# Kernel tuning notes

Hardware: AMD Instinct MI355X
Metric: run time of the kernel (lower is better)

The kernel has to match this reference:

```python
import jax, jax.numpy as jnp
import numpy as np

B, S, WD, H, STEP = 32, 512, 512, 512, 2
NG = 8  # gate order: f1, f2, f3, f4, f5, i, o, u


def setup_inputs() -> dict:
    key = jax.random.key(0)
    ks = jax.random.split(key, 12)
    std = 0.1
    word_inputs = jax.random.normal(ks[0], (B, S, WD), jnp.float32)
    position_table = jax.random.randint(ks[1], (B, S), 0, S + 1)  # 0 -> pad row
    mask = jnp.ones((B, S), jnp.int32)
    # nograd uniform(-0.05, 0.05) initial states created inside torch forward
    init_h = jax.random.uniform(ks[2], (B, S, H), jnp.float32, -0.05, 0.05)
    init_c = jax.random.uniform(ks[3], (B, S, H), jnp.float32, -0.05, 0.05)
    Wx = std * jax.random.normal(ks[4], (NG, H, H), jnp.float32)
    Wh = std * jax.random.normal(ks[5], (NG, 2 * H, H), jnp.float32)
    Wi = std * jax.random.normal(ks[6], (NG, WD, H), jnp.float32)
    Wd = std * jax.random.normal(ks[7], (NG, H, H), jnp.float32)
    Ws = std * jax.random.normal(ks[8], (NG, H, H), jnp.float32)
    b = std * jax.random.normal(ks[9], (NG, H), jnp.float32)
    gW = std * jax.random.normal(ks[10], (6, H, H), jnp.float32)  # Wxd,Whd,Wxo,Who,Wxf,Whf
    gb = std * jax.random.normal(ks[11], (3, H), jnp.float32)     # bd,bo,bf
    return dict(word_inputs=word_inputs, init_h=init_h, init_c=init_c,
                Wx=Wx, Wh=Wh, Wi=Wi, Wd=Wd, Ws=Ws, b=b, gW=gW, gb=gb,
                position_table=position_table, mask=mask, num_layers=4)


def _shift_sum_before(x, steps):
    # sum_{s=1..steps} of x right-shifted by s with zero padding at front
    out = jnp.zeros_like(x)
    for s in range(1, steps + 1):
        pad = jnp.zeros(x[:, :s].shape, x.dtype)
        out = out + jnp.concatenate([pad, x[:, :-s]], axis=1)
    return out


def _shift_sum_after(x, steps):
    out = jnp.zeros_like(x)
    for s in range(1, steps + 1):
        pad = jnp.zeros(x[:, :s].shape, x.dtype)
        out = out + jnp.concatenate([x[:, s:], pad], axis=1)
    return out


def _position_switch(x, pos):
    # prepend a zero pad row at position 0, then gather along seq dim
    x_add = jnp.concatenate([jnp.zeros_like(x[:, :1]), x], axis=1)  # [B,S+1,H]
    return jnp.take_along_axis(x_add, pos[:, :, None], axis=1)


def reference(word_inputs, init_h, init_c, Wx, Wh, Wi, Wd, Ws, b, gW, gb,
              position_table, mask, num_layers):
    maskf = mask.astype(jnp.float32)
    seq_mask = maskf[:, :, None]                         # [B,S,1]
    mask_score = (maskf * 1e25 - 1e25)[:, :, None]       # 0 where valid, -1e25 where pad
    emb = (word_inputs * seq_mask).reshape(-1, WD)       # embedding_hidden_state_pre
    h = init_h * seq_mask
    c = init_c * seq_mask
    dummy_h = jnp.mean(h, axis=1)
    dummy_c = jnp.mean(c, axis=1)
    gWxd, gWhd, gWxo, gWho, gWxf, gWhf = gW[0], gW[1], gW[2], gW[3], gW[4], gW[5]
    gbd, gbo, gbf = gb[0], gb[1], gb[2]
    for _ in range(num_layers):
        sw_h = _position_switch(h, position_table)
        sw_c = _position_switch(c, position_table)
        combined = jnp.mean(h, axis=1)                   # [B,H]
        rh = h.reshape(-1, H)                            # [B*S,H]
        td_h = jnp.broadcast_to(dummy_h[:, None], h.shape).reshape(-1, H)
        # dummy (sentence-state) node update
        gd = jax.nn.sigmoid(dummy_h @ gWxd + combined @ gWhd + gbd)
        go = jax.nn.sigmoid(dummy_h @ gWxo + combined @ gWho + gbo)
        gf = jax.nn.sigmoid(td_h @ gWxf + rh @ gWhf + gbf).reshape(h.shape) + mask_score
        scores = jax.nn.softmax(jnp.concatenate([gf, gd[:, None]], axis=1), axis=1)  # [B,S+1,H]
        dummy_c_new = jnp.sum(scores[:, :S] * c, axis=1) + scores[:, S] * dummy_c
        dummy_h_new = go * jnp.tanh(dummy_c_new)
        # neighbor window sums (before/after) for h and c
        hb = _shift_sum_before(h, STEP).reshape(-1, H)
        ha = _shift_sum_after(h, STEP).reshape(-1, H)
        cb = _shift_sum_before(c, STEP).reshape(-1, H)
        ca = _shift_sum_after(c, STEP).reshape(-1, H)
        cat = jnp.concatenate([hb, ha], axis=1)          # [B*S,2H]
        td_c = jnp.broadcast_to(dummy_c[:, None], c.shape).reshape(-1, H)
        sw_hf = sw_h.reshape(-1, H)
        sw_cf = sw_c.reshape(-1, H)
        # all 8 gate pre-activations in stacked einsums: [8,B*S,H]
        z = (jnp.einsum('nh,ghk->gnk', rh, Wx)
             + jnp.einsum('nd,gdk->gnk', cat, Wh)
             + jnp.einsum('nw,gwk->gnk', emb, Wi)
             + jnp.einsum('nh,ghk->gnk', td_h, Wd)
             + jnp.einsum('nh,ghk->gnk', sw_hf, Ws)
             + b[:, None, :])
        gates6 = jax.nn.softmax(jax.nn.sigmoid(z[:6]), axis=0)  # normalize f1..f5,i
        f1, f2, f3, f4, f5, i_t = gates6[0], gates6[1], gates6[2], gates6[3], gates6[4], gates6[5]
        o_t = jax.nn.sigmoid(z[6])
        u_t = jnp.tanh(z[7])
        cf = c.reshape(-1, H)
        c_new = f1 * cb + f2 * ca + f3 * cf + f4 * td_c + f5 * sw_cf + i_t * u_t
        h_new = o_t * jnp.tanh(c_new)
        h = h_new.reshape(B, S, H) * seq_mask
        c = c_new.reshape(B, S, H) * seq_mask
        dummy_h, dummy_c = dummy_h_new, dummy_c_new
    return h
```

## Files before the change

### kernel.cpp

```cpp
#include <hip/hip_runtime.h>
#include <cstddef>

#define Bn 32
#define Sn 512
#define Hn 512
#define Rn (Bn*Sn)
#define NLAYER 4
constexpr size_t NHe = (size_t)Rn * Hn;

typedef __attribute__((ext_vector_type(8))) _Float16 f16x8;
typedef __attribute__((ext_vector_type(4))) float f32x4;

__device__ __forceinline__ float sigf(float x) { return 1.f / (1.f + __expf(-x)); }
__device__ __forceinline__ void gl_lds16(const void* g, void* l) {
  __builtin_amdgcn_global_load_lds((const __attribute__((address_space(1))) void*)g,
                                   (__attribute__((address_space(3))) void*)l, 16, 0, 0);
}
#define VMCNT(n) asm volatile("s_waitcnt vmcnt(" #n ")" ::: "memory")

__device__ __forceinline__ int a32slot(int b, int k) {
  int kcT = k >> 5, quad = (k >> 3) & 3, j = k & 7, rg = b >> 4, l15 = b & 15;
  return ((((kcT * 2 + rg) * 4 + quad) * 16 + l15) * 8) + j;
}

__global__ void k_init(const float* __restrict__ ih, const float* __restrict__ ic,
                       const int* __restrict__ mask,
                       float* __restrict__ h, float* __restrict__ c) {
  size_t i = (size_t)blockIdx.x * blockDim.x + threadIdx.x;
  size_t n = i >> 7;
  float m = (float)mask[n];
  float4 b = ((const float4*)ih)[i];
  float4 d = ((const float4*)ic)[i];
  b.x *= m; b.y *= m; b.z *= m; b.w *= m;
  d.x *= m; d.y *= m; d.z *= m; d.w *= m;
  ((float4*)h)[i] = b; ((float4*)c)[i] = d;
}

__global__ void k_mean2(const float* __restrict__ x, const float* __restrict__ y,
                        _Float16* __restrict__ dh16, float* __restrict__ oy) {
  int idx = blockIdx.x * blockDim.x + threadIdx.x;
  int b = idx >> 9, k = idx & 511;
  const float* px = x + (size_t)b * Sn * Hn + k;
  const float* py = y + (size_t)b * Sn * Hn + k;
  float sx = 0.f, sy = 0.f;
#pragma unroll 8
  for (int t = 0; t < Sn; ++t) { sx += px[(size_t)t * Hn]; sy += py[(size_t)t * Hn]; }
  oy[idx] = sy * (1.f / Sn);
  dh16[a32slot(b, k)] = (_Float16)(sx * (1.f / Sn));
}

__global__ void k_mean1a(const float* __restrict__ x, float* __restrict__ part) {
  int b = blockIdx.x, sc = blockIdx.y;
  int k4 = threadIdx.x & 127;
  int so = threadIdx.x >> 7;
  const float4* px = (const float4*)x + ((size_t)(b * Sn + sc * 64 + so)) * 128 + k4;
  float4 s = make_float4(0.f, 0.f, 0.f, 0.f);
#pragma unroll 4
  for (int t = 0; t < 32; ++t) {
    float4 v = px[(size_t)t * 256];
    s.x += v.x; s.y += v.y; s.z += v.z; s.w += v.w;
  }
  ((float4*)part)[((size_t)(sc * 2 + so) * Bn + b) * 128 + k4] = s;
}
__global__ void k_mean1b(const float* __restrict__ part, _Float16* __restrict__ comb16) {
  int idx = blockIdx.x * blockDim.x + threadIdx.x;
  int b = idx >> 7, k4 = idx & 127;
  float4 s = make_float4(0.f, 0.f, 0.f, 0.f);
#pragma unroll
  for (int p = 0; p < 16; ++p) {
    float4 v = ((const float4*)part)[((size_t)p * Bn + b) * 128 + k4];
    s.x += v.x; s.y += v.y; s.z += v.z; s.w += v.w;
  }
  float vv[4] = {s.x, s.y, s.z, s.w};
#pragma unroll
  for (int jj = 0; jj < 4; ++jj)
    comb16[a32slot(b, k4 * 4 + jj)] = (_Float16)(vv[jj] * (1.f / Sn));
}

__global__ void k_convS(const float* __restrict__ gW, const float* __restrict__ Wd,
                        _Float16* __restrict__ Shat) {
  int kcT = blockIdx.x, nT4 = blockIdx.y, mat = blockIdx.z;
  int tid = threadIdx.x;
  const float* w = (mat < 5) ? (gW + (size_t)mat * 262144)
                             : (Wd + (size_t)(mat - 5) * 262144);
  size_t sb = ((size_t)((mat * 4 + nT4) * 16 + kcT)) * 4096;
#pragma unroll
  for (int half = 0; half < 2; ++half) {
    int st = half * 256 + tid;
    int nj = st >> 6, quad = (st >> 4) & 3, l15 = st & 15;
    int n = nT4 * 128 + nj * 16 + l15;
    int k0 = kcT * 32 + quad * 8;
    f16x8 w8;
#pragma unroll
    for (int j = 0; j < 8; ++j) w8[j] = (_Float16)w[(size_t)(k0 + j) * Hn + n];
    *(f16x8*)&Shat[sb + (size_t)st * 8] = w8;
  }
}

__global__ __launch_bounds__(256) void k_small(const _Float16* __restrict__ dh16,
                                               const _Float16* __restrict__ comb16,
                                               const _Float16* __restrict__ Shat,
                                               float* __restrict__ S) {
  const int mat = blockIdx.x, nT4 = blockIdx.y;
  const int tid = threadIdx.x;
  const int lane = tid & 63, wid = tid >> 6;
  const int quad = lane >> 4, l15 = lane & 15;
  const _Float16* A16 = (mat == 1 || mat == 3) ? comb16 : dh16;
  const _Float16* Sb = Shat + ((size_t)((mat * 4 + nT4) * 16)) * 4096;

  f32x4 acc[2][2];
#pragma unroll
  for (int rg = 0; rg < 2; ++rg)
#pragma unroll
    for (int nj = 0; nj < 2; ++nj) acc[rg][nj] = (f32x4){0.f, 0.f, 0.f, 0.f};

#pragma unroll 4
  for (int kcT = 0; kcT < 16; ++kcT) {
    f16x8 a0 = *(const f16x8*)&A16[(((kcT * 2 + 0) * 4 + quad) * 16 + l15) * 8];
    f16x8 a1 = *(const f16x8*)&A16[(((kcT * 2 + 1) * 4 + quad) * 16 + l15) * 8];
    f16x8 b0 = *(const f16x8*)&Sb[(size_t)kcT * 4096 + (((wid * 2 + 0) * 4 + quad) * 16 + l15) * 8];
    f16x8 b1 = *(const f16x8*)&Sb[(size_t)kcT * 4096 + (((wid * 2 + 1) * 4 + quad) * 16 + l15) * 8];
    acc[0][0] = __builtin_amdgcn_mfma_f32_16x16x32_f16(a0, b0, acc[0][0], 0, 0, 0);
    acc[0][1] = __builtin_amdgcn_mfma_f32_16x16x32_f16(a0, b1, acc[0][1], 0, 0, 0);
    acc[1][0] = __builtin_amdgcn_mfma_f32_16x16x32_f16(a1, b0, acc[1][0], 0, 0, 0);
    acc[1][1] = __builtin_amdgcn_mfma_f32_16x16x32_f16(a1, b1, acc[1][1], 0, 0, 0);
  }
#pragma unroll
  for (int rg = 0; rg < 2; ++rg)
#pragma unroll
    for (int nj = 0; nj < 2; ++nj)
#pragma unroll
      for (int r = 0; r < 4; ++r) {
        int brow = rg * 16 + quad * 4 + r;
        int col = nT4 * 128 + (wid * 2 + nj) * 16 + l15;
        S[(size_t)mat * 16384 + brow * 512 + col] = acc[rg][nj][r];
      }
}

__global__ void k_gates2(const float* __restrict__ S, const float* __restrict__ gb,
                         float* __restrict__ gd, float* __restrict__ go,
                         float* __restrict__ gfA) {
  int idx = blockIdx.x * blockDim.x + threadIdx.x;
  int k = idx & 511;
  gd[idx] = sigf(S[idx] + S[16384 + idx] + gb[k]);
  go[idx] = sigf(S[2 * 16384 + idx] + S[3 * 16384 + idx] + gb[512 + k]);
  gfA[idx] = S[4 * 16384 + idx] + gb[1024 + k];
}

__global__ void k_dummy2(const float* __restrict__ pnum, const float* __restrict__ pden,
                         const float* __restrict__ gd, const float* __restrict__ go,
                         const float* __restrict__ dc,
                         _Float16* __restrict__ dh16o, float* __restrict__ dc2) {
  int idx = blockIdx.x * blockDim.x + threadIdx.x;
  int b = idx >> 9, k = idx & 511;
  float ed = __expf(gd[idx]);
  float num = ed * dc[idx], den = ed;
#pragma unroll
  for (int q = 0; q < 4; ++q) {
    num += pnum[(size_t)(b * 4 + q) * 512 + k];
    den += pden[(size_t)(b * 4 + q) * 512 + k];
  }
  float d = num / den;
  dc2[idx] = d;
  dh16o[a32slot(b, k)] = (_Float16)(go[idx] * tanhf(d));
}

__global__ void k_convw(const float* __restrict__ Wx, const float* __restrict__ Wh,
                        const float* __restrict__ Wsm, const float* __restrict__ Wi,
                        _Float16* __restrict__ Bhat) {
  int kcT = blockIdx.x, nT = blockIdx.y, tg = blockIdx.z;
  int t = tg >> 3, g = tg & 7;
  const float* base;
  if (t == 0)      base = Wx  + (size_t)g * 262144;
  else if (t == 1) base = Wh  + (size_t)g * 524288;
  else if (t == 2) base = Wh  + (size_t)g * 524288 + 262144;
  else if (t == 3) base = Wsm + (size_t)g * 262144;
  else             base = Wi  + (size_t)g * 262144;
  size_t sbase = ((size_t)(t * 16 + nT) * 16 + kcT) * 8192 + (size_t)g * 1024;
  int lane = threadIdx.x;
  for (int cch = lane; cch < 128; cch += 64) {
    int ni = cch >> 6, quad = (cch >> 4) & 3, l15 = cch & 15;
    int n = nT * 32 + ni * 16 + l15;
    int k0 = kcT * 32 + quad * 8;
    f16x8 w8;
#pragma unroll
    for (int j = 0; j < 8; ++j) w8[j] = (_Float16)base[(size_t)(k0 + j) * Hn + n];
    *(f16x8*)&Bhat[sbase + (size_t)cch * 8] = w8;
  }
}

__global__ void k_convG(const float* __restrict__ gW, _Float16* __restrict__ Ghat) {
  int kcT = blockIdx.x, nT4 = blockIdx.y;
  int tid = threadIdx.x;
  const float* w = gW + (size_t)5 * Hn * Hn;
  size_t sb = ((size_t)(nT4 * 16 + kcT)) * 4096;
#pragma unroll
  for (int half = 0; half < 2; ++half) {
    int st = half * 256 + tid;
    int nj = st >> 6, quad = (st >> 4) & 3, l15 = st & 15;
    int n = nT4 * 128 + nj * 16 + l15;
    int k0 = kcT * 32 + quad * 8;
    f16x8 w8;
#pragma unroll
    for (int j = 0; j < 8; ++j) w8[j] = (_Float16)w[(size_t)(k0 + j) * Hn + n];
    *(f16x8*)&Ghat[sb + (size_t)st * 8] = w8;
  }
}

__global__ void k_prepAll(const float* __restrict__ h, const int* __restrict__ pos,
                          _Float16* __restrict__ Ahat) {
  const int mb = blockIdx.x, kcT = blockIdx.y;
  const int tid = threadIdx.x;
#pragma unroll
  for (int half = 0; half < 2; ++half) {
    int st = half * 256 + tid;
    int rg = st >> 6, quad = (st >> 4) & 3, l15 = st & 15;
    int r = mb * 128 + rg * 16 + l15;
    int srow = r & (Sn - 1);
    int k0 = kcT * 32 + quad * 8;
    const float* base = h + (size_t)r * Hn + k0;
    float v0[8], v1[8], v2[8], v3[8];
#pragma unroll
    for (int j = 0; j < 8; ++j) { v0[j] = base[j]; v1[j] = 0.f; v2[j] = 0.f; v3[j] = 0.f; }
    if (srow >= 1) { const float* p = base - Hn;
#pragma unroll
      for (int j = 0; j < 8; ++j) v1[j] += p[j]; }
    if (srow >= 2) { const float* p = base - 2 * Hn;
#pragma unroll
      for (int j = 0; j < 8; ++j) v1[j] += p[j]; }
    if (srow <= Sn - 2) { const float* p = base + Hn;
#pragma unroll
      for (int j = 0; j < 8; ++j) v2[j] += p[j]; }
    if (srow <= Sn - 3) { const float* p = base + 2 * Hn;
#pragma unroll
      for (int j = 0; j < 8; ++j) v2[j] += p[j]; }
    int pp = pos[r];
    if (pp) {
      const float* p = h + ((size_t)((r >> 9) * Sn + pp - 1)) * Hn + k0;
#pragma unroll
      for (int j = 0; j < 8; ++j) v3[j] = p[j];
    }
    size_t stoff = (size_t)st * 8;
    f16x8 o0, o1, o2, o3;
#pragma unroll
    for (int j = 0; j < 8; ++j) {
      o0[j] = (_Float16)v0[j]; o1[j] = (_Float16)v1[j];
      o2[j] = (_Float16)v2[j]; o3[j] = (_Float16)v3[j];
    }
    *(f16x8*)&Ahat[((size_t)(0 * 128 + mb) * 16 + kcT) * 4096 + stoff] = o0;
    *(f16x8*)&Ahat[((size_t)(1 * 128 + mb) * 16 + kcT) * 4096 + stoff] = o1;
    *(f16x8*)&Ahat[((size_t)(2 * 128 + mb) * 16 + kcT) * 4096 + stoff] = o2;
    *(f16x8*)&Ahat[((size_t)(3 * 128 + mb) * 16 + kcT) * 4096 + stoff] = o3;
  }
}

__global__ void k_prepW(const float* __restrict__ w, const int* __restrict__ mask,
                        _Float16* __restrict__ Ahat) {
  const int mb = blockIdx.x, kcT = blockIdx.y;
  const int tid = threadIdx.x;
  size_t sb = ((size_t)(4 * 128 + mb) * 16 + kcT) * 4096;
#pragma unroll
  for (int half = 0; half < 2; ++half) {
    int st = half * 256 + tid;
    int rg = st >> 6, quad = (st >> 4) & 3, l15 = st & 15;
    int r = mb * 128 + rg * 16 + l15;
    int k0 = kcT * 32 + quad * 8;
    float mf = (float)mask[r];
    const float* base = w + (size_t)r * Hn + k0;
    f16x8 o8;
#pragma unroll
    for (int j = 0; j < 8; ++j) o8[j] = (_Float16)(base[j] * mf);
    *(f16x8*)&Ahat[sb + (size_t)st * 8] = o8;
  }
}

__global__ __launch_bounds__(256, 2) void k_gemm1d(const _Float16* __restrict__ Ahat,
                                                   const _Float16* __restrict__ Ghat,
                                                   const float* __restrict__ gfA,
                                                   const float* __restrict__ cbuf,
                                                   const int* __restrict__ mask,
                                                   float* __restrict__ pnum,
                                                   float* __restrict__ pden) {
  __shared__ _Float16 As[2][4096];
  __shared__ _Float16 Bs[2][4096];
  __shared__ float red[4][2][128];
  const int tid = threadIdx.x;
  const int mb = blockIdx.x, nT4 = blockIdx.y;
  const int lane = tid & 63, wid = tid >> 6;
  const int quad = lane >> 4, l15 = lane & 15;
  const int afo0 = (((wid * 2 + 0) * 4 + quad) * 16 + l15) * 8;
  const int afo1 = (((wid * 2 + 1) * 4 + quad) * 16 + l15) * 8;

  f32x4 acc[2][8];
#pragma unroll
  for (int mi = 0; mi < 2; ++mi)
#pragma unroll
    for (int nj = 0; nj < 8; ++nj) acc[mi][nj] = (f32x4){0.f, 0.f, 0.f, 0.f};

  auto stage = [&](int buf, int kcT) {
    const int4* sa = (const int4*)Ahat + ((size_t)(mb * 16 + kcT) << 9);
    const int4* sbp = (const int4*)Ghat + ((size_t)(nT4 * 16 + kcT) << 9);
#pragma unroll
    for (int q = 0; q < 2; ++q) {
      gl_lds16(sa + q * 256 + tid, &As[buf][(q * 256 + tid) * 8]);
      gl_lds16(sbp + q * 256 + tid, &Bs[buf][(q * 256 + tid) * 8]);
    }
  };

  stage(0, 0);
  __syncthreads();
#pragma unroll 1
  for (int kcT = 0; kcT < 16; ++kcT) {
    const int cur = kcT & 1;
    if (kcT < 15) stage(cur ^ 1, kcT + 1);
    f16x8 a0 = *(const f16x8*)&As[cur][afo0];
    f16x8 a1 = *(const f16x8*)&As[cur][afo1];
#pragma unroll
    for (int nj = 0; nj < 8; ++nj) {
      f16x8 bh = *(const f16x8*)&Bs[cur][((nj * 4 + quad) * 16 + l15) * 8];
      acc[0][nj] = __builtin_amdgcn_mfma_f32_16x16x32_f16(a0, bh, acc[0][nj], 0, 0, 0);
      acc[1][nj] = __builtin_amdgcn_mfma_f32_16x16x32_f16(a1, bh, acc[1][nj], 0, 0, 0);
    }
    __syncthreads();
  }

  const int bb = mb >> 2;
  float gfa[8], nsum[8], dsum[8];
#pragma unroll
  for (int nj = 0; nj < 8; ++nj) {
    gfa[nj] = gfA[bb * 512 + nT4 * 128 + nj * 16 + l15];
    nsum[nj] = 0.f; dsum[nj] = 0.f;
  }
#pragma unroll
  for (int mi = 0; mi < 2; ++mi) {
#pragma unroll
    for (int r = 0; r < 4; ++r) {
      int row = mb * 128 + wid * 32 + mi * 16 + quad * 4 + r;
      float mf = (float)mask[row];
      const float* crow = cbuf + (size_t)row * 512 + nT4 * 128 + l15;
#pragma unroll
      for (int nj = 0; nj < 8; ++nj) {
        float e = __expf(sigf(acc[mi][nj][r] + gfa[nj])) * mf;
        nsum[nj] += e * crow[nj * 16];
        dsum[nj] += e;
      }
    }
  }
#pragma unroll
  for (int nj = 0; nj < 8; ++nj) {
    nsum[nj] += __shfl_xor(nsum[nj], 16);
    nsum[nj] += __shfl_xor(nsum[nj], 32);
    dsum[nj] += __shfl_xor(dsum[nj], 16);
    dsum[nj] += __shfl_xor(dsum[nj], 32);
  }
  if (quad == 0) {
#pragma unroll
    for (int nj = 0; nj < 8; ++nj) {
      red[wid][0][nj * 16 + l15] = nsum[nj];
      red[wid][1][nj * 16 + l15] = dsum[nj];
    }
  }
  __syncthreads();
  {
    int cc = tid & 127, which = tid >> 7;
    float v = red[0][which][cc] + red[1][which][cc] + red[2][which][cc] + red[3][which][cc];
    float* dst = which ? pden : pnum;
    dst[(size_t)mb * 512 + nT4 * 128 + cc] = v;
  }
}

__global__ __launch_bounds__(512, 2) void k_mega(
    const float* __restrict__ c,
    const _Float16* __restrict__ Ahat, const _Float16* __restrict__ Bhat,
    const int* __restrict__ pos, const int* __restrict__ mask,
    const float* __restrict__ dc, const float* __restrict__ dWd,
    const float* __restrict__ bias,
    float* __restrict__ hout, float* __restrict__ cout) {
  __shared__ _Float16 As[2][16384];
  __shared__ _Float16 Bs[2][16384];

  const int tid = threadIdx.x;
  const int id = blockIdx.x;
  const int xcd = id & 7;
  const int loc = id >> 3;
  const int mt = xcd * 8 + (loc >> 4);
  const int nT = loc & 15;
  const int m0 = mt * 256;
  const int n0 = nT * 32;
  const int bb = m0 >> 9;

  const int lane = tid & 63, wid = tid >> 6;
  const int quad = lane >> 4, l15 = lane & 15;
  const int row_grp = wid >> 1;
  const int col_half = wid & 1;
  const int mb2 = row_grp >> 1;
  const int rg0 = (row_grp & 1) * 4;

  const int afoA0 = (mb2 * 4096) + ((rg0 * 4 + quad) * 16 + l15) * 8;
  const int afoA1 = (2 * 4096 + mb2 * 4096) + ((rg0 * 4 + quad) * 16 + l15) * 8;
  const int bfo = col_half * 512 + quad * 128 + l15 * 8;

  f32x4 acc[8][4];
#pragma unroll
  for (int g = 0; g < 8; ++g)
#pragma unroll
    for (int mi = 0; mi < 4; ++mi) acc[g][mi] = (f32x4){0.f, 0.f, 0.f, 0.f};

  auto stageA = [&](int buf, int kt2) {
    const int t = kt2 >> 3, kc2 = (kt2 & 7) * 2;
#pragma unroll
    for (int kk = 0; kk < 2; ++kk)
#pragma unroll
      for (int m2 = 0; m2 < 2; ++m2) {
        const int4* src = (const int4*)Ahat +
            ((size_t)((t * 128 + mt * 2 + m2) * 16 + kc2 + kk)) * 512;
        gl_lds16(src + tid, &As[buf][(kk * 2 + m2) * 4096 + tid * 8]);
      }
#pragma unroll
    for (int kk = 0; kk < 2; ++kk) {
      const int4* srcb = (const int4*)Bhat +
          ((size_t)((t * 16 + nT) * 16 + kc2 + kk)) * 1024;
      gl_lds16(srcb + tid, &Bs[buf][kk * 8192 + tid * 8]);
    }
  };
  auto stageB = [&](int buf, int kt2) {
    const int t = kt2 >> 3, kc2 = (kt2 & 7) * 2;
#pragma unroll
    for (int kk = 0; kk < 2; ++kk) {
      const int4* srcb = (const int4*)Bhat +
          ((size_t)((t * 16 + nT) * 16 + kc2 + kk)) * 1024 + 512;
      gl_lds16(srcb + tid, &Bs[buf][kk * 8192 + 4096 + tid * 8]);
    }
  };

  stageA(0, 0);
  stageB(0, 0);

#pragma unroll 1
  for (int kt = 0; kt < 40; ++kt) {
    const int cur = kt & 1;
    const int nbuf = cur ^ 1;
    VMCNT(2);
    __builtin_amdgcn_s_barrier();
    f16x8 a[4][2], b[4];
#pragma unroll
    for (int mi = 0; mi < 4; ++mi) {
      a[mi][0] = *(const f16x8*)&As[cur][afoA0 + mi * 512];
      a[mi][1] = *(const f16x8*)&As[cur][afoA1 + mi * 512];
    }
#pragma unroll
    for (int g = 0; g < 4; ++g) b[g] = *(const f16x8*)&Bs[cur][g * 1024 + bfo];
    if (kt < 39) stageA(nbuf, kt + 1);
    asm volatile("s_waitcnt lgkmcnt(0)" ::: "memory");
    __builtin_amdgcn_sched_barrier(0);
    __builtin_amdgcn_s_setprio(1);
#pragma unroll
    for (int g = 0; g < 4; ++g) {
#pragma unroll
      for (int mi = 0; mi < 4; ++mi)
        acc[g][mi] = __builtin_amdgcn_mfma_f32_16x16x32_f16(a[mi][0], b[g], acc[g][mi], 0, 0, 0);
    }
    f16x8 b1[4];
#pragma unroll
    for (int g = 0; g < 4; ++g) b1[g] = *(const f16x8*)&Bs[cur][8192 + g * 1024 + bfo];
    asm volatile("s_waitcnt lgkmcnt(0)" ::: "memory");
    __builtin_amdgcn_sched_barrier(0);
#pragma unroll
    for (int g = 0; g < 4; ++g) {
#pragma unroll
      for (int mi = 0; mi < 4; ++mi)
        acc[g][mi] = __builtin_amdgcn_mfma_f32_16x16x32_f16(a[mi][1], b1[g], acc[g][mi], 0, 0, 0);
    }
    __builtin_amdgcn_s_setprio(0);
    if (kt < 39) { VMCNT(6); }
    else         { VMCNT(0); }
    __builtin_amdgcn_s_barrier();
    f16x8 c0[4], c1[4];
#pragma unroll
    for (int g = 0; g < 4; ++g) {
      c0[g] = *(const f16x8*)&Bs[cur][4096 + g * 1024 + bfo];
      c1[g] = *(const f16x8*)&Bs[cur][8192 + 4096 + g * 1024 + bfo];
    }
    if (kt < 39) stageB(nbuf, kt + 1);
    asm volatile("s_waitcnt lgkmcnt(0)" ::: "memory");
    __builtin_amdgcn_sched_barrier(0);
    __builtin_amdgcn_s_setprio(1);
#pragma unroll
    for (int g = 0; g < 4; ++g) {
#pragma unroll
      for (int mi = 0; mi < 4; ++mi)
        acc[4 + g][mi] = __builtin_amdgcn_mfma_f32_16x16x32_f16(a[mi][0], c0[g], acc[4 + g][mi], 0, 0, 0);
    }
#pragma unroll
    for (int g = 0; g < 4; ++g) {
#pragma unroll
      for (int mi = 0; mi < 4; ++mi)
        acc[4 + g][mi] = __builtin_amdgcn_mfma_f32_16x16x32_f16(a[mi][1], c1[g], acc[4 + g][mi], 0, 0, 0);
    }
    __builtin_amdgcn_s_setprio(0);
    __builtin_amdgcn_s_barrier();
  }

  const int col = n0 + col_half * 16 + l15;
  const float tdcv = dc[bb * Hn + col];
  float biasr[8], dwdr[8];
#pragma unroll
  for (int g = 0; g < 8; ++g) {
    biasr[g] = bias[g * Hn + col];
    dwdr[g] = dWd[((size_t)g * Bn + bb) * Hn + col];
  }

#pragma unroll
  for (int mi = 0; mi < 4; ++mi) {
#pragma unroll
    for (int r = 0; r < 4; ++r) {
      const int row = m0 + row_grp * 64 + mi * 16 + quad * 4 + r;
      const int srow = row & (Sn - 1);
      const float mf = (float)mask[row];
      const int pp = pos[row];
      const size_t rb = (size_t)row * Hn;
      float cf = c[rb + col];
      float cb = 0.f, ca = 0.f;
      if (srow >= 1) cb = c[rb - Hn + col];
      if (srow >= 2) cb += c[rb - 2 * Hn + col];
      if (srow <= Sn - 2) ca = c[rb + Hn + col];
      if (srow <= Sn - 3) ca += c[rb + 2 * Hn + col];
      float sw = pp ? c[((size_t)(bb * Sn + pp - 1)) * Hn + col] : 0.f;
      float z[8];
#pragma unroll
      for (int g = 0; g < 8; ++g)
        z[g] = acc[g][mi][r] + biasr[g] + dwdr[g];
      float e0 = __expf(sigf(z[0]));
      float e1 = __expf(sigf(z[1]));
      float e2 = __expf(sigf(z[2]));
      float e3 = __expf(sigf(z[3]));
      float e4 = __expf(sigf(z[4]));
      float e5 = __expf(sigf(z[5]));
      float inv = 1.f / (e0 + e1 + e2 + e3 + e4 + e5);
      float o = sigf(z[6]);
      float u = tanhf(z[7]);
      float cn = inv * (e0 * cb + e1 * ca + e2 * cf + e3 * tdcv + e4 * sw + e5 * u);
      cout[rb + col] = cn * mf;
      hout[rb + col] = o * tanhf(cn) * mf;
    }
  }
}

extern "C" void kernel_launch(void* const* d_in, const int* in_sizes, int n_in,
                              void* d_out, int out_size, void* d_ws, size_t ws_size,
                              hipStream_t stream) {
  (void)in_sizes; (void)n_in; (void)out_size; (void)ws_size;
  const float* word   = (const float*)d_in[0];
  const float* init_h = (const float*)d_in[1];
  const float* init_c = (const float*)d_in[2];
  const float* Wx     = (const float*)d_in[3];
  const float* Wh     = (const float*)d_in[4];
  const float* Wi     = (const float*)d_in[5];
  const float* Wdm    = (const float*)d_in[6];
  const float* Wsm    = (const float*)d_in[7];
  const float* bias   = (const float*)d_in[8];
  const float* gW     = (const float*)d_in[9];
  const float* gb     = (const float*)d_in[10];
  const int*   pos    = (const int*)d_in[11];
  const int*   mask   = (const int*)d_in[12];

  float* ws = (float*)d_ws;
  size_t off = 0;
  auto alloc = [&](size_t nel) { float* p = ws + off; off += nel; return p; };
  float* cA   = alloc(NHe);
  float* cB   = alloc(NHe);
  float* hS   = alloc(NHe);
  _Float16* Ahat = (_Float16*)alloc(5 * NHe / 2);
  _Float16* Bhat = (_Float16*)alloc(5 * 8 * 512 * 512 / 2);
  _Float16* Ghat = (_Float16*)alloc(512 * 512 / 2);
  _Float16* Shat = (_Float16*)alloc(13 * 512 * 512 / 2);
  float* S    = alloc(13 * 16384);
  float* part = alloc(16 * Bn * Hn);
  float* pnum = alloc(128 * 512);
  float* pden = alloc(128 * 512);
  _Float16* dh16A = (_Float16*)alloc(8192);
  _Float16* dh16B = (_Float16*)alloc(8192);
  _Float16* comb16 = (_Float16*)alloc(8192);
  float* dc   = alloc(Bn * Hn);
  float* dc2  = alloc(Bn * Hn);
  float* gd   = alloc(Bn * Hn);
  float* go   = alloc(Bn * Hn);
  float* gfA  = alloc(Bn * Hn);

  dim3 blk(256);
  int g4 = (int)(NHe / 4 / 256);
  int gbh = (Bn * Hn) / 256;

  k_convw<<<dim3(16, 16, 40), dim3(64), 0, stream>>>(Wx, Wh, Wsm, Wi, Bhat);
  k_convG<<<dim3(16, 4), blk, 0, stream>>>(gW, Ghat);
  k_convS<<<dim3(16, 4, 13), blk, 0, stream>>>(gW, Wdm, Shat);
  k_prepW<<<dim3(128, 16), blk, 0, stream>>>(word, mask, Ahat);
  k_init<<<g4, blk, 0, stream>>>(init_h, init_c, mask, hS, cA);
  k_mean2<<<gbh, blk, 0, stream>>>(hS, cA, dh16A, dc);

  float* ccur = cA; float* cnxt = cB;
  _Float16* dhc = dh16A; _Float16* dhn = dh16B;
  for (int l = 0; l < NLAYER; ++l) {
    k_prepAll<<<dim3(128, 16), blk, 0, stream>>>(hS, pos, Ahat);
    k_mean1a<<<dim3(Bn, 8), blk, 0, stream>>>(hS, part);
    k_mean1b<<<16, blk, 0, stream>>>(part, comb16);
    k_small<<<dim3(13, 4), blk, 0, stream>>>(dhc, comb16, Shat, S);
    k_gates2<<<gbh, blk, 0, stream>>>(S, gb, gd, go, gfA);
    k_gemm1d<<<dim3(128, 4), blk, 0, stream>>>(Ahat, Ghat, gfA, ccur, mask, pnum, pden);
    k_dummy2<<<gbh, blk, 0, stream>>>(pnum, pden, gd, go, dc, dhn, dc2);

    float* hout = (l == NLAYER - 1) ? (float*)d_out : hS;
    k_mega<<<dim3(1024), dim3(512), 0, stream>>>(
        ccur, Ahat, Bhat, pos, mask, dc, S + (size_t)5 * 16384, bias, hout, cnxt);

    float* t1;
    t1 = ccur; ccur = cnxt; cnxt = t1;
    t1 = dc; dc = dc2; dc2 = t1;
    _Float16* t2 = dhc; dhc = dhn; dhn = t2;
  }
}
```

Measured before the change: 1.884 ms.

## Switch mega GEMM to triple-buffered single-K-chunk pipeline with one barrier per step

Replaces the double-buffered loop, which handled two K chunks per iteration and split A and B staging across several barriers, with a triple-buffered ring that handles one K chunk per iteration. Each step waits on loads, takes one barrier, prefetches the chunk two steps ahead, then interleaves B-fragment LDS reads with MFMAs. The aim is fewer barriers and deeper prefetch so load latency is hidden better. Launch bounds drop to one block per SIMD-pair, and the explicit priority and scheduling hints are removed, which may lower occupancy and loosen the MFMA issue ordering.

```diff
diff --git a/kernel.cpp b/kernel.cpp
--- a/kernel.cpp
+++ b/kernel.cpp
@@ -369,15 +369,15 @@
   }
 }
 
-__global__ __launch_bounds__(512, 2) void k_mega(
+__global__ __launch_bounds__(512, 1) void k_mega(
     const float* __restrict__ c,
     const _Float16* __restrict__ Ahat, const _Float16* __restrict__ Bhat,
     const int* __restrict__ pos, const int* __restrict__ mask,
     const float* __restrict__ dc, const float* __restrict__ dWd,
     const float* __restrict__ bias,
     float* __restrict__ hout, float* __restrict__ cout) {
-  __shared__ _Float16 As[2][16384];
-  __shared__ _Float16 Bs[2][16384];
+  __shared__ _Float16 As[3][8192];
+  __shared__ _Float16 Bs[3][8192];
 
   const int tid = threadIdx.x;
   const int id = blockIdx.x;
@@ -396,8 +396,7 @@
   const int mb2 = row_grp >> 1;
   const int rg0 = (row_grp & 1) * 4;
 
-  const int afoA0 = (mb2 * 4096) + ((rg0 * 4 + quad) * 16 + l15) * 8;
-  const int afoA1 = (2 * 4096 + mb2 * 4096) + ((rg0 * 4 + quad) * 16 + l15) * 8;
+  const int afo = mb2 * 4096 + rg0 * 512 + quad * 128 + l15 * 8;
   const int bfo = col_half * 512 + quad * 128 + l15 * 8;
 
   f32x4 acc[8][4];
@@ -406,99 +405,48 @@
 #pragma unroll
     for (int mi = 0; mi < 4; ++mi) acc[g][mi] = (f32x4){0.f, 0.f, 0.f, 0.f};
 
-  auto stageA = [&](int buf, int kt2) {
-    const int t = kt2 >> 3, kc2 = (kt2 & 7) * 2;
-#pragma unroll
-    for (int kk = 0; kk < 2; ++kk)
-#pragma unroll
-      for (int m2 = 0; m2 < 2; ++m2) {
-        const int4* src = (const int4*)Ahat +
-            ((size_t)((t * 128 + mt * 2 + m2) * 16 + kc2 + kk)) * 512;
-        gl_lds16(src + tid, &As[buf][(kk * 2 + m2) * 4096 + tid * 8]);
-      }
-#pragma unroll
-    for (int kk = 0; kk < 2; ++kk) {
-      const int4* srcb = (const int4*)Bhat +
-          ((size_t)((t * 16 + nT) * 16 + kc2 + kk)) * 1024;
-      gl_lds16(srcb + tid, &Bs[buf][kk * 8192 + tid * 8]);
-    }
+  auto stage = [&](int buf, int cn) {
+    const int t = cn >> 4, kcT = cn & 15;
+#pragma unroll
+    for (int m2 = 0; m2 < 2; ++m2) {
+      const int4* src = (const int4*)Ahat +
+          ((size_t)((t * 128 + mt * 2 + m2) * 16 + kcT)) * 512;
+      gl_lds16(src + tid, &As[buf][m2 * 4096 + tid * 8]);
+    }
+    const int4* sbp = (const int4*)Bhat + ((size_t)((t * 16 + nT) * 16 + kcT)) * 1024;
+    gl_lds16(sbp + tid, &Bs[buf][tid * 8]);
+    gl_lds16(sbp + 512 + tid, &Bs[buf][4096 + tid * 8]);
   };
-  auto stageB = [&](int buf, int kt2) {
-    const int t = kt2 >> 3, kc2 = (kt2 & 7) * 2;
-#pragma unroll
-    for (int kk = 0; kk < 2; ++kk) {
-      const int4* srcb = (const int4*)Bhat +
-          ((size_t)((t * 16 + nT) * 16 + kc2 + kk)) * 1024 + 512;
-      gl_lds16(srcb + tid, &Bs[buf][kk * 8192 + 4096 + tid * 8]);
-    }
-  };
-
-  stageA(0, 0);
-  stageB(0, 0);
-
+
+  stage(0, 0);
+  stage(1, 1);
+  int cur = 0;
 #pragma unroll 1
-  for (int kt = 0; kt < 40; ++kt) {
-    const int cur = kt & 1;
-    const int nbuf = cur ^ 1;
-    VMCNT(2);
-    __builtin_amdgcn_s_barrier();
-    f16x8 a[4][2], b[4];
-#pragma unroll
-    for (int mi = 0; mi < 4; ++mi) {
-      a[mi][0] = *(const f16x8*)&As[cur][afoA0 + mi * 512];
-      a[mi][1] = *(const f16x8*)&As[cur][afoA1 + mi * 512];
-    }
-#pragma unroll
-    for (int g = 0; g < 4; ++g) b[g] = *(const f16x8*)&Bs[cur][g * 1024 + bfo];
-    if (kt < 39) stageA(nbuf, kt + 1);
-    asm volatile("s_waitcnt lgkmcnt(0)" ::: "memory");
-    __builtin_amdgcn_sched_barrier(0);
-    __builtin_amdgcn_s_setprio(1);
-#pragma unroll
-    for (int g = 0; g < 4; ++g) {
-#pragma unroll
-      for (int mi = 0; mi < 4; ++mi)
-        acc[g][mi] = __builtin_amdgcn_mfma_f32_16x16x32_f16(a[mi][0], b[g], acc[g][mi], 0, 0, 0);
-    }
-    f16x8 b1[4];
-#pragma unroll
-    for (int g = 0; g < 4; ++g) b1[g] = *(const f16x8*)&Bs[cur][8192 + g * 1024 + bfo];
-    asm volatile("s_waitcnt lgkmcnt(0)" ::: "memory");
-    __builtin_amdgcn_sched_barrier(0);
-#pragma unroll
-    for (int g = 0; g < 4; ++g) {
-#pragma unroll
-      for (int mi = 0; mi < 4; ++mi)
-        acc[g][mi] = __builtin_amdgcn_mfma_f32_16x16x32_f16(a[mi][1], b1[g], acc[g][mi], 0, 0, 0);
-    }
-    __builtin_amdgcn_s_setprio(0);
-    if (kt < 39) { VMCNT(6); }
+  for (int kt = 0; kt < 80; ++kt) {
+    if (kt < 79) { VMCNT(4); }
     else         { VMCNT(0); }
     __builtin_amdgcn_s_barrier();
-    f16x8 c0[4], c1[4];
-#pragma unroll
-    for (int g = 0; g < 4; ++g) {
-      c0[g] = *(const f16x8*)&Bs[cur][4096 + g * 1024 + bfo];
-      c1[g] = *(const f16x8*)&Bs[cur][8192 + 4096 + g * 1024 + bfo];
-    }
-    if (kt < 39) stageB(nbuf, kt + 1);
+    asm volatile("" ::: "memory");
+    if (kt + 2 < 80) {
+      int nn = (cur == 0) ? 2 : cur - 1;
+      stage(nn, kt + 2);
+    }
+    const _Float16* Ab = &As[cur][afo];
+    const _Float16* Bb = &Bs[cur][bfo];
+    f16x8 a0 = *(const f16x8*)&Ab[0];
+    f16x8 a1 = *(const f16x8*)&Ab[512];
+    f16x8 a2 = *(const f16x8*)&Ab[1024];
+    f16x8 a3 = *(const f16x8*)&Ab[1536];
+#pragma unroll
+    for (int g = 0; g < 8; ++g) {
+      f16x8 bg = *(const f16x8*)&Bb[g * 1024];
+      acc[g][0] = __builtin_amdgcn_mfma_f32_16x16x32_f16(a0, bg, acc[g][0], 0, 0, 0);
+      acc[g][1] = __builtin_amdgcn_mfma_f32_16x16x32_f16(a1, bg, acc[g][1], 0, 0, 0);
+      acc[g][2] = __builtin_amdgcn_mfma_f32_16x16x32_f16(a2, bg, acc[g][2], 0, 0, 0);
+      acc[g][3] = __builtin_amdgcn_mfma_f32_16x16x32_f16(a3, bg, acc[g][3], 0, 0, 0);
+    }
     asm volatile("s_waitcnt lgkmcnt(0)" ::: "memory");
-    __builtin_amdgcn_sched_barrier(0);
-    __builtin_amdgcn_s_setprio(1);
-#pragma unroll
-    for (int g = 0; g < 4; ++g) {
-#pragma unroll
-      for (int mi = 0; mi < 4; ++mi)
-        acc[4 + g][mi] = __builtin_amdgcn_mfma_f32_16x16x32_f16(a[mi][0], c0[g], acc[4 + g][mi], 0, 0, 0);
-    }
-#pragma unroll
-    for (int g = 0; g < 4; ++g) {
-#pragma unroll
-      for (int mi = 0; mi < 4; ++mi)
-        acc[4 + g][mi] = __builtin_amdgcn_mfma_f32_16x16x32_f16(a[mi][1], c1[g], acc[4 + g][mi], 0, 0, 0);
-    }
-    __builtin_amdgcn_s_setprio(0);
-    __builtin_amdgcn_s_barrier();
+    cur = (cur == 2) ? 0 : cur + 1;
   }
 
   const int col = n0 + col_half * 16 + l15;
```

New measurement: 2.178 ms. 1.16x slower.
